# Kernel optimization log

Hardware: AMD Instinct MI355X
Metric: run time of the kernel (lower is better)

Reference implementation:

```python
import jax, jax.numpy as jnp
import numpy as np

N_SRC0, N_FTRS, N_HID, N_CLS = 200000, 128, 1500, 64
E0, E1 = 1600000, 500000
RES0, RES1 = 50000, 10000


def sage_conv(x, src, tgt, res_size, W_root, W_neigh, b):
    # mean aggregation of neighbor (source) features onto the first res_size target nodes
    msg = x[src]                                              # [E, F] gather
    summed = jax.ops.segment_sum(msg, tgt, num_segments=res_size)   # [res, F]
    cnt = jax.ops.segment_sum(jnp.ones((src.shape[0],), x.dtype), tgt, num_segments=res_size)
    mean = summed / jnp.maximum(cnt, 1.0)[:, None]
    return x[:res_size] @ W_root + mean @ W_neigh + b


def setup_inputs() -> dict:
    key = jax.random.key(0)
    ks = jax.random.split(key, 12)
    x = jax.random.normal(ks[0], (N_SRC0, N_FTRS), dtype=jnp.float32)
    edge_src0 = jax.random.randint(ks[1], (E0,), 0, N_SRC0)
    edge_tgt0 = jax.random.randint(ks[2], (E0,), 0, RES0)
    edge_src1 = jax.random.randint(ks[3], (E1,), 0, RES0)
    edge_tgt1 = jax.random.randint(ks[4], (E1,), 0, RES1)
    s1 = 1.0 / np.sqrt(N_FTRS)
    s2 = 1.0 / np.sqrt(N_HID)
    W1_root = jax.random.uniform(ks[5], (N_FTRS, N_HID), jnp.float32, -s1, s1)
    W1_neigh = jax.random.uniform(ks[6], (N_FTRS, N_HID), jnp.float32, -s1, s1)
    b1 = jax.random.uniform(ks[7], (N_HID,), jnp.float32, -s1, s1)
    W2_root = jax.random.uniform(ks[8], (N_HID, N_CLS), jnp.float32, -s2, s2)
    W2_neigh = jax.random.uniform(ks[9], (N_HID, N_CLS), jnp.float32, -s2, s2)
    b2 = jax.random.uniform(ks[10], (N_CLS,), jnp.float32, -s2, s2)
    return {
        "x": x,
        "W1_root": W1_root, "W1_neigh": W1_neigh, "b1": b1,
        "W2_root": W2_root, "W2_neigh": W2_neigh, "b2": b2,
        "edge_src0": edge_src0, "edge_tgt0": edge_tgt0,
        "edge_src1": edge_src1, "edge_tgt1": edge_tgt1,
        "res0": RES0, "res1": RES1,
    }


def reference(x, W1_root, W1_neigh, b1, W2_root, W2_neigh, b2,
              edge_src0, edge_tgt0, edge_src1, edge_tgt1, res0, res1):
    h = sage_conv(x, edge_src0, edge_tgt0, res0, W1_root, W1_neigh, b1)  # [res0, H]
    h = jax.nn.relu(h)
    # dropout p=0.5 is identity in eval mode
    out = sage_conv(h, edge_src1, edge_tgt1, res1, W2_root, W2_neigh, b2)  # [res1, C]
    return jax.nn.log_softmax(out, axis=1)
```

## Files before the change

### kernel.cpp

```cpp
#include <hip/hip_runtime.h>
#include <hip/hip_bf16.h>
#include <cstdint>
#include <cstddef>

#define NSRC   200000
#define NF     128
#define NHID   1500
#define NHIDP  1536
#define NCLS   64
#define E0N    1600000
#define E1N    500000
#define RES0   50000
#define RES1   10000

#define CH     4096
#define NCH0   ((E0N + CH - 1) / CH)
#define NCH1   ((E1N + CH - 1) / CH)
#define NB0    ((RES0 + 255) / 256)
#define NB1    ((RES1 + 255) / 256)

#define PREP_BLOCKS  ((256 * NHIDP + 128 * NHIDP + NHIDP + 255) / 256)
#define COPYX_BLOCKS ((NSRC * NF) / (256 * 8))

typedef __bf16 bf16x8 __attribute__((ext_vector_type(8)));
typedef float  f32x4  __attribute__((ext_vector_type(4)));
typedef unsigned short u16x8 __attribute__((ext_vector_type(8)));
typedef unsigned int u32;
typedef unsigned long long u64;

__device__ __forceinline__ unsigned short f2bf(float f) {
    union { float f; unsigned u; } v; v.f = f;
    unsigned r = v.u + 0x7fffu + ((v.u >> 16) & 1u);
    return (unsigned short)(r >> 16);
}

__device__ __forceinline__ void lds_dma16(const void* g, void* lds) {
    __builtin_amdgcn_global_load_lds(
        (const __attribute__((address_space(1))) unsigned int*)g,
        (__attribute__((address_space(3))) unsigned int*)lds, 16, 0, 0);
}

__global__ __launch_bounds__(256) void setup_kernel(
        const float* __restrict__ x, unsigned short* __restrict__ xbf,
        const float* __restrict__ W1r, const float* __restrict__ W1n,
        const float* __restrict__ b1,
        const float* __restrict__ W2r, const float* __restrict__ W2n,
        unsigned short* __restrict__ WcatT, unsigned short* __restrict__ W2catT,
        float* __restrict__ b1e) {
    int bid = blockIdx.x;
    if (bid < PREP_BLOCKS) {
        int id = bid * 256 + threadIdx.x;
        if (id < 256 * NHIDP) {
            int n = id >> 8, k = id & 255;
            float v = 0.f;
            if (n < NHID) v = (k < NF) ? W1r[k * NHID + n] : W1n[(k - NF) * NHID + n];
            WcatT[n * 256 + k] = f2bf(v);
        } else {
            int id2 = id - 256 * NHIDP;
            if (id2 < 128 * NHIDP) {
                int n = id2 / NHIDP, k = id2 % NHIDP;
                float v = 0.f;
                if (k < NHID) v = (n < 64) ? W2n[k * 64 + n] : W2r[k * 64 + (n - 64)];
                W2catT[n * NHIDP + k] = f2bf(v);
            } else {
                int c = id2 - 128 * NHIDP;
                if (c < NHIDP) b1e[c] = (c < NHID) ? b1[c] : 0.f;
            }
        }
    } else {
        size_t i = ((size_t)(bid - PREP_BLOCKS) * 256 + threadIdx.x) * 8;
        const float4* s = (const float4*)(x + i);
        float4 a = s[0], b = s[1];
        u16x8 o;
        o[0] = f2bf(a.x); o[1] = f2bf(a.y); o[2] = f2bf(a.z); o[3] = f2bf(a.w);
        o[4] = f2bf(b.x); o[5] = f2bf(b.y); o[6] = f2bf(b.z); o[7] = f2bf(b.w);
        *(u16x8*)(xbf + i) = o;
    }
}

__device__ __forceinline__ void p1a_body(const int* __restrict__ tgt, int n,
                                         int nb, u32* __restrict__ H, int c) {
    __shared__ u32 lhist[256];
    int tid = threadIdx.x;
    lhist[tid] = 0;
    __syncthreads();
#pragma unroll
    for (int it = 0; it < CH / 256; ++it) {
        int i = c * CH + it * 256 + tid;
        if (i < n) atomicAdd(&lhist[((u32)tgt[i]) >> 8], 1u);
    }
    __syncthreads();
    if (tid < nb) H[c * nb + tid] = lhist[tid];
}

__global__ __launch_bounds__(256) void p1a_both_kernel(
        const int* __restrict__ t0, const int* __restrict__ t1,
        u32* __restrict__ H1, u32* __restrict__ H2) {
    int b = blockIdx.x;
    if (b < NCH0) p1a_body(t0, E0N, NB0, H1, b);
    else          p1a_body(t1, E1N, NB1, H2, b - NCH0);
}

__device__ __forceinline__ void bscan_body(const u32* __restrict__ H,
                                           int nch, int nb, int b,
                                           u32* __restrict__ base_rel,
                                           u32* __restrict__ Bsum) {
    __shared__ u32 part[512];
    int t = threadIdx.x;
    part[t] = (t < nch) ? H[t * nb + b] : 0u;
    __syncthreads();
    for (int d = 1; d < 512; d <<= 1) {
        u32 v = part[t];
        u32 add = (t >= d) ? part[t - d] : 0u;
        __syncthreads();
        part[t] = v + add;
        __syncthreads();
    }
    if (t < nch) base_rel[t * nb + b] = (t == 0) ? 0u : part[t - 1];
    if (t == 0) Bsum[b] = part[nch - 1];
}

__global__ __launch_bounds__(512) void bscan_both_kernel(
        const u32* __restrict__ H1, u32* __restrict__ base1, u32* __restrict__ Bsum1,
        const u32* __restrict__ H2, u32* __restrict__ base2, u32* __restrict__ Bsum2) {
    int b = blockIdx.x;
    if (b < NB0) bscan_body(H1, NCH0, NB0, b, base1, Bsum1);
    else         bscan_body(H2, NCH1, NB1, b - NB0, base2, Bsum2);
}

__global__ __launch_bounds__(256) void boff_kernel(const u32* __restrict__ Bsum1,
                                                   u32* __restrict__ boff1, int nb1,
                                                   const u32* __restrict__ Bsum2,
                                                   u32* __restrict__ boff2, int nb2) {
    const u32* B = blockIdx.x ? Bsum2 : Bsum1;
    u32* O = blockIdx.x ? boff2 : boff1;
    int nb = blockIdx.x ? nb2 : nb1;
    __shared__ u32 part[256];
    int t = threadIdx.x;
    part[t] = (t < nb) ? B[t] : 0u;
    __syncthreads();
    for (int d = 1; d < 256; d <<= 1) {
        u32 v = part[t];
        u32 add = (t >= d) ? part[t - d] : 0u;
        __syncthreads();
        part[t] = v + add;
        __syncthreads();
    }
    if (t < nb) O[t] = (t == 0) ? 0u : part[t - 1];
}

__device__ __forceinline__ void p1b_body(const int* __restrict__ src,
                                         const int* __restrict__ tgt, int n,
                                         int nb, const u32* __restrict__ base_rel,
                                         const u32* __restrict__ boff,
                                         u64* __restrict__ bucketed, int c) {
    __shared__ u32 lcur[256];
    __shared__ u32 lbase[256];
    int tid = threadIdx.x;
    lcur[tid] = 0;
    if (tid < nb) lbase[tid] = base_rel[c * nb + tid] + boff[tid];
    __syncthreads();
#pragma unroll
    for (int it = 0; it < CH / 256; ++it) {
        int i = c * CH + it * 256 + tid;
        if (i < n) {
            u32 t = (u32)tgt[i];
            u32 s = (u32)src[i];
            u32 b = t >> 8;
            u32 r = atomicAdd(&lcur[b], 1u);
            bucketed[lbase[b] + r] = ((u64)t << 32) | (u64)s;
        }
    }
}

__global__ __launch_bounds__(256) void p1b_both_kernel(
        const int* __restrict__ s0, const int* __restrict__ t0,
        const u32* __restrict__ base1, const u32* __restrict__ boff1,
        u64* __restrict__ bkt1,
        const int* __restrict__ s1, const int* __restrict__ t1,
        const u32* __restrict__ base2, const u32* __restrict__ boff2,
        u64* __restrict__ bkt2) {
    int b = blockIdx.x;
    if (b < NCH0) p1b_body(s0, t0, E0N, NB0, base1, boff1, bkt1, b);
    else          p1b_body(s1, t1, E1N, NB1, base2, boff2, bkt2, b - NCH0);
}

__device__ __forceinline__ void p2_body(const u64* __restrict__ bucketed,
                                        const u32* __restrict__ boff,
                                        int nb, int res, int etot,
                                        int* __restrict__ csr,
                                        u32* __restrict__ off_out,
                                        u32* __restrict__ cnt_out, int b) {
    __shared__ u32 lhist[256];
    __shared__ u32 part[256];
    __shared__ u32 cur[256];
    int tid = threadIdx.x;
    u32 start = boff[b];
    u32 end = (b == nb - 1) ? (u32)etot : boff[b + 1];
    u32 count = end - start;
    if (tid < 256) lhist[tid] = 0;
    __syncthreads();
    for (u32 i = tid; i < count; i += 1024) {
        u32 t = (u32)(bucketed[start + i] >> 32);
        atomicAdd(&lhist[t & 255u], 1u);
    }
    __syncthreads();
    if (tid < 256) part[tid] = lhist[tid];
    __syncthreads();
    for (int d = 1; d < 256; d <<= 1) {
        u32 v = (tid < 256) ? part[tid] : 0u;
        u32 add = (tid >= d && tid < 256) ? part[tid - d] : 0u;
        __syncthreads();
        if (tid < 256) part[tid] = v + add;
        __syncthreads();
    }
    if (tid < 256) {
        u32 excl = (tid == 0) ? 0u : part[tid - 1];
        cur[tid] = excl;
        int tg = (b << 8) + tid;
        if (tg < res) {
            off_out[tg] = start + excl;
            cnt_out[tg] = lhist[tid];
        }
    }
    __syncthreads();
    for (u32 i = tid; i < count; i += 1024) {
        u64 pr = bucketed[start + i];
        u32 lt = ((u32)(pr >> 32)) & 255u;
        u32 r = atomicAdd(&cur[lt], 1u);
        csr[start + r] = (int)(u32)pr;
    }
}

__global__ __launch_bounds__(1024) void p2_both_kernel(
        const u64* __restrict__ bkt1, const u32* __restrict__ boff1,
        int* __restrict__ csr1, u32* __restrict__ off1, u32* __restrict__ cnt1,
        const u64* __restrict__ bkt2, const u32* __restrict__ boff2,
        int* __restrict__ csr2, u32* __restrict__ off2, u32* __restrict__ cnt2) {
    int b = blockIdx.x;
    if (b < NB0) p2_body(bkt1, boff1, NB0, RES0, E0N, csr1, off1, cnt1, b);
    else         p2_body(bkt2, boff2, NB1, RES1, E1N, csr2, off2, cnt2, b - NB0);
}

__global__ __launch_bounds__(256) void agg1_csr_kernel(
        const u32* __restrict__ xb32, const int* __restrict__ csr,
        const u32* __restrict__ off, const u32* __restrict__ cnt,
        u32* __restrict__ mean1_32) {
    int row = blockIdx.x * 4 + (threadIdx.x >> 6);
    int lane = threadIdx.x & 63;
    if (row >= RES0) return;
    u32 base = off[row], deg = cnt[row];
    float x0 = 0.f, y0 = 0.f, x1 = 0.f, y1 = 0.f;
    float x2 = 0.f, y2 = 0.f, x3 = 0.f, y3 = 0.f;
    u32 e = 0;
    for (; e + 4 <= deg; e += 4) {
        int s0 = csr[base + e], s1 = csr[base + e + 1];
        int s2 = csr[base + e + 2], s3 = csr[base + e + 3];
        u32 w0 = xb32[(size_t)s0 * 64 + lane];
        u32 w1 = xb32[(size_t)s1 * 64 + lane];
        u32 w2 = xb32[(size_t)s2 * 64 + lane];
        u32 w3 = xb32[(size_t)s3 * 64 + lane];
        union { u32 u; float f; } a, b;
        a.u = w0 << 16; b.u = w0 & 0xffff0000u; x0 += a.f; y0 += b.f;
        a.u = w1 << 16; b.u = w1 & 0xffff0000u; x1 += a.f; y1 += b.f;
        a.u = w2 << 16; b.u = w2 & 0xffff0000u; x2 += a.f; y2 += b.f;
        a.u = w3 << 16; b.u = w3 & 0xffff0000u; x3 += a.f; y3 += b.f;
    }
    for (; e < deg; ++e) {
        u32 w = xb32[(size_t)csr[base + e] * 64 + lane];
        union { u32 u; float f; } a, b;
        a.u = w << 16; b.u = w & 0xffff0000u; x0 += a.f; y0 += b.f;
    }
    float inv = 1.0f / fmaxf((float)deg, 1.0f);
    float mx = ((x0 + x1) + (x2 + x3)) * inv;
    float my = ((y0 + y1) + (y2 + y3)) * inv;
    mean1_32[(size_t)row * 64 + lane] = (u32)f2bf(mx) | ((u32)f2bf(my) << 16);
}

__global__ __launch_bounds__(256, 2) void fused_gemm_kernel(
        const unsigned short* __restrict__ xbf, const unsigned short* __restrict__ mean1,
        const unsigned short* __restrict__ WcatT, const float* __restrict__ b1e,
        const unsigned short* __restrict__ W2catT,
        float* __restrict__ pp0, float* __restrict__ pp1) {
    __shared__ __align__(16) unsigned short As0[128 * 32];
    __shared__ __align__(16) unsigned short As1[128 * 32];
    __shared__ __align__(16) unsigned short Bs0[128 * 32];
    __shared__ __align__(16) unsigned short Bs1[128 * 32];
    __shared__ __align__(16) unsigned short Ht[128 * 136];

    int m0 = blockIdx.x * 128;
    int jb = blockIdx.y * 6;
    float* pout = blockIdx.y ? pp1 : pp0;
    int tid = threadIdx.x;
    int lane = tid & 63, wid = tid >> 6;
    int wm = wid >> 1, wn = wid & 1;
    int quad = lane >> 4, l15 = lane & 15;

    f32x4 pacc[4][4] = {};

    for (int j = jb; j < jb + 6; ++j) {
        f32x4 hacc[4][4] = {};
        for (int kk = 0; kk < 256; kk += 64) {
#pragma unroll
            for (int kh = 0; kh < 2; ++kh) {
                int ksel = kk + kh * 32;
                const unsigned short* src = (ksel < 128)
                    ? xbf + (size_t)m0 * NF + ksel
                    : mean1 + (size_t)m0 * NF + (ksel - 128);
                unsigned short* dst = kh ? As1 : As0;
#pragma unroll
                for (int ci = 0; ci < 2; ++ci) {
                    int cb = ci * 256 + wid * 64;
                    int chunk = cb + lane;
                    int n = chunk >> 2, kc = chunk & 3;
                    lds_dma16(src + (size_t)n * NF + kc * 8, &dst[cb * 8]);
                }
            }
#pragma unroll
            for (int kh = 0; kh < 2; ++kh) {
                int ksel = kk + kh * 32;
                const unsigned short* src = WcatT + (size_t)(j * 128) * 256 + ksel;
                unsigned short* dst = kh ? Bs1 : Bs0;
#pragma unroll
                for (int ci = 0; ci < 2; ++ci) {
                    int cb = ci * 256 + wid * 64;
                    int chunk = cb + lane;
                    int n = chunk >> 2, kc = chunk & 3;
                    lds_dma16(src + (size_t)n * 256 + kc * 8, &dst[cb * 8]);
                }
            }
            __syncthreads();
#pragma unroll
            for (int kh = 0; kh < 2; ++kh) {
                const unsigned short* Asb = kh ? As1 : As0;
                const unsigned short* Bsb = kh ? Bs1 : Bs0;
                bf16x8 a[4], b[4];
#pragma unroll
                for (int mi = 0; mi < 4; ++mi)
                    a[mi] = *(const bf16x8*)(&Asb[(wm * 64 + mi * 16 + l15) * 32 + quad * 8]);
#pragma unroll
                for (int ni = 0; ni < 4; ++ni)
                    b[ni] = *(const bf16x8*)(&Bsb[(wn * 64 + ni * 16 + l15) * 32 + quad * 8]);
#pragma unroll
                for (int mi = 0; mi < 4; ++mi)
#pragma unroll
                    for (int ni = 0; ni < 4; ++ni)
                        hacc[mi][ni] = __builtin_amdgcn_mfma_f32_16x16x32_bf16(a[mi], b[ni], hacc[mi][ni], 0, 0, 0);
            }
            __syncthreads();
        }
#pragma unroll
        for (int ni = 0; ni < 4; ++ni) {
            int lc = wn * 64 + ni * 16 + l15;
            float bv = b1e[j * 128 + lc];
#pragma unroll
            for (int mi = 0; mi < 4; ++mi) {
#pragma unroll
                for (int r = 0; r < 4; ++r) {
                    int row = wm * 64 + mi * 16 + quad * 4 + r;
                    Ht[row * 136 + lc] = f2bf(fmaxf(hacc[mi][ni][r] + bv, 0.f));
                }
            }
        }
        __syncthreads();
#pragma unroll
        for (int kk2 = 0; kk2 < 128; kk2 += 32) {
            bf16x8 a2[4], b2[4];
#pragma unroll
            for (int mi = 0; mi < 4; ++mi)
                a2[mi] = *(const bf16x8*)(&Ht[(wm * 64 + mi * 16 + l15) * 136 + kk2 + quad * 8]);
#pragma unroll
            for (int ni = 0; ni < 4; ++ni)
                b2[ni] = *(const bf16x8*)(W2catT + (size_t)(wn * 64 + ni * 16 + l15) * NHIDP
                                          + j * 128 + kk2 + quad * 8);
#pragma unroll
            for (int mi = 0; mi < 4; ++mi)
#pragma unroll
                for (int ni = 0; ni < 4; ++ni)
                    pacc[mi][ni] = __builtin_amdgcn_mfma_f32_16x16x32_bf16(a2[mi], b2[ni], pacc[mi][ni], 0, 0, 0);
        }
        __syncthreads();
    }

#pragma unroll
    for (int ni = 0; ni < 4; ++ni) {
        int gc = wn * 64 + ni * 16 + l15;
#pragma unroll
        for (int mi = 0; mi < 4; ++mi) {
#pragma unroll
            for (int r = 0; r < 4; ++r) {
                int gr = m0 + wm * 64 + mi * 16 + quad * 4 + r;
                if (gr < RES0) pout[(size_t)gr * 128 + gc] = pacc[mi][ni][r];
            }
        }
    }
}

__global__ __launch_bounds__(256) void padd_kernel(float* __restrict__ pp0,
                                                   const float* __restrict__ pp1) {
    size_t i = (size_t)blockIdx.x * 256 + threadIdx.x;
    f32x4 a = ((const f32x4*)pp0)[i];
    f32x4 b = ((const f32x4*)pp1)[i];
    ((f32x4*)pp0)[i] = a + b;
}

__global__ __launch_bounds__(64) void final_csr_kernel(
        const float* __restrict__ p, const int* __restrict__ csr,
        const u32* __restrict__ off, const u32* __restrict__ cnt,
        const float* __restrict__ b2, float* __restrict__ out) {
    int row = blockIdx.x;
    int c = threadIdx.x;
    u32 base = off[row], deg = cnt[row];
    float a0 = 0.f, a1 = 0.f, a2 = 0.f, a3 = 0.f;
    u32 e = 0;
    for (; e + 4 <= deg; e += 4) {
        int s0 = csr[base + e], s1 = csr[base + e + 1];
        int s2 = csr[base + e + 2], s3 = csr[base + e + 3];
        a0 += p[(size_t)s0 * 128 + c];
        a1 += p[(size_t)s1 * 128 + c];
        a2 += p[(size_t)s2 * 128 + c];
        a3 += p[(size_t)s3 * 128 + c];
    }
    for (; e < deg; ++e) a0 += p[(size_t)csr[base + e] * 128 + c];
    float mean = ((a0 + a1) + (a2 + a3)) / fmaxf((float)deg, 1.0f);
    float v = p[(size_t)row * 128 + 64 + c] + mean + b2[c];
    float m = v;
#pragma unroll
    for (int o = 32; o > 0; o >>= 1) m = fmaxf(m, __shfl_xor(m, o, 64));
    float ex = expf(v - m);
    float s = ex;
#pragma unroll
    for (int o = 32; o > 0; o >>= 1) s += __shfl_xor(s, o, 64);
    out[(size_t)row * 64 + c] = v - m - logf(s);
}

extern "C" void kernel_launch(void* const* d_in, const int* in_sizes, int n_in,
                              void* d_out, int out_size, void* d_ws, size_t ws_size,
                              hipStream_t stream) {
    const float* x   = (const float*)d_in[0];
    const float* W1r = (const float*)d_in[1];
    const float* W1n = (const float*)d_in[2];
    const float* b1  = (const float*)d_in[3];
    const float* W2r = (const float*)d_in[4];
    const float* W2n = (const float*)d_in[5];
    const float* b2  = (const float*)d_in[6];
    const int* es0 = (const int*)d_in[7];
    const int* et0 = (const int*)d_in[8];
    const int* es1 = (const int*)d_in[9];
    const int* et1 = (const int*)d_in[10];
    float* out = (float*)d_out;

    char* ws = (char*)d_ws;
    const size_t PPBYTES = (size_t)RES0 * 128 * 4;
    float* pp1 = (float*)ws;
    size_t o0 = 0;
    auto alloc0 = [&](size_t bytes) {
        void* ptr = ws + o0;
        o0 = (o0 + bytes + 255) & ~(size_t)255;
        return ptr;
    };
    u64* bkt1  = (u64*)alloc0((size_t)E0N * 8);
    u64* bkt2  = (u64*)alloc0((size_t)E1N * 8);
    int* csr1  = (int*)alloc0((size_t)E0N * 4);
    u32* H1    = (u32*)alloc0((size_t)NCH0 * NB0 * 4);
    u32* base1 = (u32*)alloc0((size_t)NCH0 * NB0 * 4);
    u32* H2    = (u32*)alloc0((size_t)NCH1 * NB1 * 4);
    u32* base2 = (u32*)alloc0((size_t)NCH1 * NB1 * 4);
    u32* Bsum1 = (u32*)alloc0((size_t)NB0 * 4);
    u32* Bsum2 = (u32*)alloc0((size_t)NB1 * 4);
    u32* boff1 = (u32*)alloc0((size_t)NB0 * 4);
    u32* boff2 = (u32*)alloc0((size_t)NB1 * 4);
    u32* off1  = (u32*)alloc0((size_t)RES0 * 4);
    u32* cnt1  = (u32*)alloc0((size_t)RES0 * 4);

    size_t off_ = PPBYTES;
    auto alloc = [&](size_t bytes) {
        void* ptr = ws + off_;
        off_ = (off_ + bytes + 255) & ~(size_t)255;
        return ptr;
    };
    int* csr2  = (int*)alloc((size_t)E1N * 4);
    u32* off2  = (u32*)alloc((size_t)RES1 * 4);
    u32* cnt2  = (u32*)alloc((size_t)RES1 * 4);
    unsigned short* xbf    = (unsigned short*)alloc((size_t)NSRC * NF * 2);
    unsigned short* mean1  = (unsigned short*)alloc((size_t)(RES0 + 128) * NF * 2);
    unsigned short* WcatT  = (unsigned short*)alloc((size_t)NHIDP * 256 * 2);
    unsigned short* W2catT = (unsigned short*)alloc((size_t)128 * NHIDP * 2);
    float*          b1e    = (float*)alloc((size_t)NHIDP * 4);
    float*          pp0    = (float*)alloc(PPBYTES);

    setup_kernel<<<PREP_BLOCKS + COPYX_BLOCKS, 256, 0, stream>>>(
        x, xbf, W1r, W1n, b1, W2r, W2n, WcatT, W2catT, b1e);

    p1a_both_kernel<<<NCH0 + NCH1, 256, 0, stream>>>(et0, et1, H1, H2);
    bscan_both_kernel<<<NB0 + NB1, 512, 0, stream>>>(H1, base1, Bsum1, H2, base2, Bsum2);
    boff_kernel<<<2, 256, 0, stream>>>(Bsum1, boff1, NB0, Bsum2, boff2, NB1);
    p1b_both_kernel<<<NCH0 + NCH1, 256, 0, stream>>>(
        es0, et0, base1, boff1, bkt1, es1, et1, base2, boff2, bkt2);
    p2_both_kernel<<<NB0 + NB1, 1024, 0, stream>>>(
        bkt1, boff1, csr1, off1, cnt1, bkt2, boff2, csr2, off2, cnt2);

    agg1_csr_kernel<<<(RES0 + 3) / 4, 256, 0, stream>>>(
        (const u32*)xbf, csr1, off1, cnt1, (u32*)mean1);

    fused_gemm_kernel<<<dim3((RES0 + 127) / 128, 2), 256, 0, stream>>>(
        xbf, mean1, WcatT, b1e, W2catT, pp0, pp1);

    padd_kernel<<<(RES0 * 128 / 4 + 255) / 256, 256, 0, stream>>>(pp0, pp1);

    final_csr_kernel<<<RES1, 64, 0, stream>>>(pp0, csr2, off2, cnt2, b2, out);
}
```

Baseline: 460.8 us.

## Double-buffer GEMM K-chunks and vectorize epilogue via swapped MFMA operands

Restructures the fused GEMM's inner loop into a double-buffered pipeline: it prefetches the next 32-wide K chunk into the alternate LDS buffer while computing the current one, and stages the first chunk of the next column tile during the second GEMM. The MFMA operands are swapped so each lane holds four consecutive columns, which allows float4 bias loads, ushort4 stores into Ht and float4 global output stores. This aims to hide global-to-LDS latency and cut the number of barriers and scalar stores. The cost is one barrier per 32-wide chunk instead of per 64, and correctness depends on the prefetch into As[0] after the Ht barrier not racing with other readers.

```diff
diff --git a/kernel.cpp b/kernel.cpp
--- a/kernel.cpp
+++ b/kernel.cpp
@@ -277,15 +277,38 @@
     mean1_32[(size_t)row * 64 + lane] = (u32)f2bf(mx) | ((u32)f2bf(my) << 16);
 }
 
+__device__ __forceinline__ void stage_chunk(
+        const unsigned short* __restrict__ xbf, const unsigned short* __restrict__ mean1,
+        const unsigned short* __restrict__ WcatT, int m0, int j, int kt,
+        unsigned short* As, unsigned short* Bs, int wid, int lane) {
+    int ksel = kt * 32;
+    const unsigned short* srcA = (ksel < 128)
+        ? xbf + (size_t)m0 * NF + ksel
+        : mean1 + (size_t)m0 * NF + (ksel - 128);
+#pragma unroll
+    for (int ci = 0; ci < 2; ++ci) {
+        int cb = ci * 256 + wid * 64;
+        int chunk = cb + lane;
+        int n = chunk >> 2, kc = chunk & 3;
+        lds_dma16(srcA + (size_t)n * NF + kc * 8, &As[cb * 8]);
+    }
+    const unsigned short* srcB = WcatT + (size_t)(j * 128) * 256 + ksel;
+#pragma unroll
+    for (int ci = 0; ci < 2; ++ci) {
+        int cb = ci * 256 + wid * 64;
+        int chunk = cb + lane;
+        int n = chunk >> 2, kc = chunk & 3;
+        lds_dma16(srcB + (size_t)n * 256 + kc * 8, &Bs[cb * 8]);
+    }
+}
+
 __global__ __launch_bounds__(256, 2) void fused_gemm_kernel(
         const unsigned short* __restrict__ xbf, const unsigned short* __restrict__ mean1,
         const unsigned short* __restrict__ WcatT, const float* __restrict__ b1e,
         const unsigned short* __restrict__ W2catT,
         float* __restrict__ pp0, float* __restrict__ pp1) {
-    __shared__ __align__(16) unsigned short As0[128 * 32];
-    __shared__ __align__(16) unsigned short As1[128 * 32];
-    __shared__ __align__(16) unsigned short Bs0[128 * 32];
-    __shared__ __align__(16) unsigned short Bs1[128 * 32];
+    __shared__ __align__(16) unsigned short As[2][128 * 32];
+    __shared__ __align__(16) unsigned short Bs[2][128 * 32];
     __shared__ __align__(16) unsigned short Ht[128 * 136];
 
     int m0 = blockIdx.x * 128;
@@ -298,71 +321,49 @@
 
     f32x4 pacc[4][4] = {};
 
+    stage_chunk(xbf, mean1, WcatT, m0, jb, 0, As[0], Bs[0], wid, lane);
+
     for (int j = jb; j < jb + 6; ++j) {
         f32x4 hacc[4][4] = {};
-        for (int kk = 0; kk < 256; kk += 64) {
-#pragma unroll
-            for (int kh = 0; kh < 2; ++kh) {
-                int ksel = kk + kh * 32;
-                const unsigned short* src = (ksel < 128)
-                    ? xbf + (size_t)m0 * NF + ksel
-                    : mean1 + (size_t)m0 * NF + (ksel - 128);
-                unsigned short* dst = kh ? As1 : As0;
-#pragma unroll
-                for (int ci = 0; ci < 2; ++ci) {
-                    int cb = ci * 256 + wid * 64;
-                    int chunk = cb + lane;
-                    int n = chunk >> 2, kc = chunk & 3;
-                    lds_dma16(src + (size_t)n * NF + kc * 8, &dst[cb * 8]);
-                }
+#pragma unroll
+        for (int kt = 0; kt < 8; ++kt) {
+            __syncthreads();
+            if (kt < 7)
+                stage_chunk(xbf, mean1, WcatT, m0, j, kt + 1,
+                            As[(kt + 1) & 1], Bs[(kt + 1) & 1], wid, lane);
+            const unsigned short* Asb = As[kt & 1];
+            const unsigned short* Bsb = Bs[kt & 1];
+            bf16x8 a[4], b[4];
+#pragma unroll
+            for (int mi = 0; mi < 4; ++mi)
+                a[mi] = *(const bf16x8*)(&Asb[(wm * 64 + mi * 16 + l15) * 32 + quad * 8]);
+#pragma unroll
+            for (int ni = 0; ni < 4; ++ni)
+                b[ni] = *(const bf16x8*)(&Bsb[(wn * 64 + ni * 16 + l15) * 32 + quad * 8]);
+#pragma unroll
+            for (int mi = 0; mi < 4; ++mi)
+#pragma unroll
+                for (int ni = 0; ni < 4; ++ni)
+                    hacc[mi][ni] = __builtin_amdgcn_mfma_f32_16x16x32_bf16(b[ni], a[mi], hacc[mi][ni], 0, 0, 0);
+        }
+#pragma unroll
+        for (int ni = 0; ni < 4; ++ni) {
+            int n0 = wn * 64 + ni * 16 + quad * 4;
+            float4 bv = *(const float4*)(b1e + j * 128 + n0);
+#pragma unroll
+            for (int mi = 0; mi < 4; ++mi) {
+                int m = wm * 64 + mi * 16 + l15;
+                ushort4 o;
+                o.x = f2bf(fmaxf(hacc[mi][ni][0] + bv.x, 0.f));
+                o.y = f2bf(fmaxf(hacc[mi][ni][1] + bv.y, 0.f));
+                o.z = f2bf(fmaxf(hacc[mi][ni][2] + bv.z, 0.f));
+                o.w = f2bf(fmaxf(hacc[mi][ni][3] + bv.w, 0.f));
+                *(ushort4*)(&Ht[m * 136 + n0]) = o;
             }
-#pragma unroll
-            for (int kh = 0; kh < 2; ++kh) {
-                int ksel = kk + kh * 32;
-                const unsigned short* src = WcatT + (size_t)(j * 128) * 256 + ksel;
-                unsigned short* dst = kh ? Bs1 : Bs0;
-#pragma unroll
-                for (int ci = 0; ci < 2; ++ci) {
-                    int cb = ci * 256 + wid * 64;
-                    int chunk = cb + lane;
-                    int n = chunk >> 2, kc = chunk & 3;
-                    lds_dma16(src + (size_t)n * 256 + kc * 8, &dst[cb * 8]);
-                }
-            }
-            __syncthreads();
-#pragma unroll
-            for (int kh = 0; kh < 2; ++kh) {
-                const unsigned short* Asb = kh ? As1 : As0;
-                const unsigned short* Bsb = kh ? Bs1 : Bs0;
-                bf16x8 a[4], b[4];
-#pragma unroll
-                for (int mi = 0; mi < 4; ++mi)
-                    a[mi] = *(const bf16x8*)(&Asb[(wm * 64 + mi * 16 + l15) * 32 + quad * 8]);
-#pragma unroll
-                for (int ni = 0; ni < 4; ++ni)
-                    b[ni] = *(const bf16x8*)(&Bsb[(wn * 64 + ni * 16 + l15) * 32 + quad * 8]);
-#pragma unroll
-                for (int mi = 0; mi < 4; ++mi)
-#pragma unroll
-                    for (int ni = 0; ni < 4; ++ni)
-                        hacc[mi][ni] = __builtin_amdgcn_mfma_f32_16x16x32_bf16(a[mi], b[ni], hacc[mi][ni], 0, 0, 0);
-            }
-            __syncthreads();
-        }
-#pragma unroll
-        for (int ni = 0; ni < 4; ++ni) {
-            int lc = wn * 64 + ni * 16 + l15;
-            float bv = b1e[j * 128 + lc];
-#pragma unroll
-            for (int mi = 0; mi < 4; ++mi) {
-#pragma unroll
-                for (int r = 0; r < 4; ++r) {
-                    int row = wm * 64 + mi * 16 + quad * 4 + r;
-                    Ht[row * 136 + lc] = f2bf(fmaxf(hacc[mi][ni][r] + bv, 0.f));
-                }
-            }
-        }
-        __syncthreads();
+        }
+        __syncthreads();
+        if (j + 1 < jb + 6)
+            stage_chunk(xbf, mean1, WcatT, m0, j + 1, 0, As[0], Bs[0], wid, lane);
 #pragma unroll
         for (int kk2 = 0; kk2 < 128; kk2 += 32) {
             bf16x8 a2[4], b2[4];
@@ -377,20 +378,18 @@
             for (int mi = 0; mi < 4; ++mi)
 #pragma unroll
                 for (int ni = 0; ni < 4; ++ni)
-                    pacc[mi][ni] = __builtin_amdgcn_mfma_f32_16x16x32_bf16(a2[mi], b2[ni], pacc[mi][ni], 0, 0, 0);
-        }
-        __syncthreads();
-    }
-
-#pragma unroll
-    for (int ni = 0; ni < 4; ++ni) {
-        int gc = wn * 64 + ni * 16 + l15;
-#pragma unroll
-        for (int mi = 0; mi < 4; ++mi) {
-#pragma unroll
-            for (int r = 0; r < 4; ++r) {
-                int gr = m0 + wm * 64 + mi * 16 + quad * 4 + r;
-                if (gr < RES0) pout[(size_t)gr * 128 + gc] = pacc[mi][ni][r];
+                    pacc[mi][ni] = __builtin_amdgcn_mfma_f32_16x16x32_bf16(b2[ni], a2[mi], pacc[mi][ni], 0, 0, 0);
+        }
+    }
+
+#pragma unroll
+    for (int mi = 0; mi < 4; ++mi) {
+        int gr = m0 + wm * 64 + mi * 16 + l15;
+        if (gr < RES0) {
+#pragma unroll
+            for (int ni = 0; ni < 4; ++ni) {
+                int gc0 = wn * 64 + ni * 16 + quad * 4;
+                *(float4*)(&pout[(size_t)gr * 128 + gc0]) = *(float4*)(&pacc[mi][ni]);
             }
         }
     }
```

Measured after the change: 464.8 us. About the same (+0.9%).
